# Optimization experiments

Hardware: AMD Instinct MI355X
Metric: run time of the kernel (lower is better)

## Reference

```python
import jax, jax.numpy as jnp
import numpy as np

GRID_SIZE = 5
SPLINE_ORDER = 3
GRID_RANGE = (-1.0, 1.0)
NUM_COEF = GRID_SIZE + SPLINE_ORDER  # 8


def make_grid(in_features):
    h = (GRID_RANGE[1] - GRID_RANGE[0]) / GRID_SIZE
    g = jnp.arange(-SPLINE_ORDER, GRID_SIZE + SPLINE_ORDER + 1, dtype=jnp.float32) * h + GRID_RANGE[0]
    return jnp.broadcast_to(g, (in_features, g.shape[0]))  # (in, grid_size + 2*order + 1)


def b_splines(x, grid):
    # x: (N, in); grid: (in, G). Cox-de Boor recursion -> (N, in, grid_size+order)
    xe = x[..., None]
    bases = ((xe >= grid[:, :-1]) & (xe < grid[:, 1:])).astype(x.dtype)
    for k in range(1, SPLINE_ORDER + 1):
        left = (xe - grid[:, : -(k + 1)]) / (grid[:, k:-1] - grid[:, : -(k + 1)])
        right = (grid[:, k + 1:] - xe) / (grid[:, k + 1:] - grid[:, 1:-k])
        bases = left * bases[..., :-1] + right * bases[..., 1:]
    return bases


def kan_linear(x, grid, base_w, spline_w, scaler):
    # base path: silu(x) @ base_w.T   (base_w: (out, in))
    base_out = jnp.einsum('ni,oi->no', jax.nn.silu(x), base_w)
    # spline path: flatten basis and scaled spline weights into one GEMM
    basis = b_splines(x, grid)                       # (N, in, 8)
    sw = spline_w * scaler[..., None]                # (out, in, 8)
    spline_out = jnp.einsum('nik,oik->no', basis, sw)
    return base_out + spline_out


def setup_inputs() -> dict:
    key = jax.random.key(0)
    ks = jax.random.split(key, 8)
    d = 1024
    dff = 4 * d
    n_tok = 4096
    s = 0.02
    return {
        'x': jax.random.normal(ks[0], (n_tok, d), dtype=jnp.float32),
        'base_w1': jax.random.normal(ks[1], (dff, d), dtype=jnp.float32) * s,
        'spline_w1': jax.random.normal(ks[2], (dff, d, NUM_COEF), dtype=jnp.float32) * s,
        'scaler1': jnp.ones((dff, d), dtype=jnp.float32),
        'base_w2': jax.random.normal(ks[3], (d, dff), dtype=jnp.float32) * s,
        'spline_w2': jax.random.normal(ks[4], (d, dff, NUM_COEF), dtype=jnp.float32) * s,
        'scaler2': jnp.ones((d, dff), dtype=jnp.float32),
        'grid1': make_grid(d),
        'grid2': make_grid(dff),
    }


def reference(x, base_w1, spline_w1, scaler1, base_w2, spline_w2, scaler2, grid1, grid2):
    h = kan_linear(x, grid1, base_w1, spline_w1, scaler1)
    h = jax.nn.gelu(h, approximate=False)  # torch nn.GELU default (erf)
    h = kan_linear(h, grid2, base_w2, spline_w2, scaler2)
    # Dropout(0.1) is identity in eval mode
    return h + x
```

## Files before the change

kernel.cpp:

```cpp
#include <hip/hip_runtime.h>
#include <hip/hip_fp16.h>

typedef _Float16 half_t;
typedef __attribute__((ext_vector_type(8))) _Float16 half8;
typedef __attribute__((ext_vector_type(4))) float f32x4;

#define AS1 __attribute__((address_space(1)))
#define AS3 __attribute__((address_space(3)))

__device__ __forceinline__ void gload16(const half_t* g, half_t* l) {
  __builtin_amdgcn_global_load_lds((const AS1 void*)g, (AS3 void*)l, 16, 0, 0);
}

__device__ __forceinline__ void bspline8u(float x, float out[8]) {
  float g[12];
#pragma unroll
  for (int j = 0; j < 12; ++j) g[j] = (float)(j - 3) * 0.4f - 1.0f;
  float b[11];
#pragma unroll
  for (int j = 0; j < 11; ++j)
    b[j] = (x >= g[j] && x < g[j + 1]) ? 1.0f : 0.0f;
#pragma unroll
  for (int k = 1; k <= 3; ++k) {
#pragma unroll
    for (int j = 0; j + k < 11; ++j) {
      float rl = 1.0f / (g[j + k] - g[j]);
      float rr = 1.0f / (g[j + k + 1] - g[j + 1]);
      b[j] = ((x - g[j]) * rl) * b[j] + ((g[j + k + 1] - x) * rr) * b[j + 1];
    }
  }
#pragma unroll
  for (int j = 0; j < 8; ++j) out[j] = b[j];
}

__global__ void wconv_kernel(const float* __restrict__ bw, const float* __restrict__ sw,
                             const float* __restrict__ sc, half_t* __restrict__ W,
                             int ibits, int ldw) {
  int idx = blockIdx.x * 256 + threadIdx.x;
  int o = idx >> ibits;
  int i = idx & ((1 << ibits) - 1);
  int c = i >> 10;
  int il = i & 1023;
  float b = bw[idx];
  float scv = sc[idx];
  const float4* svp = (const float4*)sw;
  float4 s0 = svp[(size_t)idx * 2];
  float4 s1 = svp[(size_t)idx * 2 + 1];
  half_t* wrow = W + (size_t)o * ldw + c * 9216;
  wrow[il] = (half_t)b;
  half8 hv;
  hv[0] = (half_t)(s0.x * scv); hv[1] = (half_t)(s0.y * scv);
  hv[2] = (half_t)(s0.z * scv); hv[3] = (half_t)(s0.w * scv);
  hv[4] = (half_t)(s1.x * scv); hv[5] = (half_t)(s1.y * scv);
  hv[6] = (half_t)(s1.z * scv); hv[7] = (half_t)(s1.w * scv);
  *(half8*)&wrow[1024 + il * 8] = hv;
}

template <typename ST>
__global__ void expand_kernel(const ST* __restrict__ src, half_t* __restrict__ dst,
                              int Isrc, int i0, int dsub, int kexp) {
  int idx = blockIdx.x * 256 + threadIdx.x;
  int n = idx >> 10;
  int il = idx & 1023;
  float v = (float)src[(size_t)n * Isrc + i0 + il];
  float bs[8];
  bspline8u(v, bs);
  half_t* drow = dst + (size_t)n * kexp + (size_t)dsub * 9216;
  drow[il] = (half_t)(v / (1.0f + expf(-v)));
  half8 hb;
#pragma unroll
  for (int k = 0; k < 8; ++k) hb[k] = (half_t)bs[k];
  *(half8*)&drow[1024 + il * 8] = hb;
}

#define STA(c, t, h)                                                          \
  {                                                                           \
    int r0_ = wid * 8 + (h) * 64;                                             \
    const half_t* g_ = Abase + (size_t)(r0_ + srow) * ldkA +                  \
                       (size_t)(t) * 64 + scol;                               \
    gload16(g_, &As[c][r0_ * 64]);                                            \
    gload16(g_ + (size_t)128 * ldkA, &As[c][(r0_ + 128) * 64]);               \
  }
#define STB(c, t, h)                                                          \
  {                                                                           \
    int r0_ = (wid >> 2) * 64 + (wid & 3) * 8 + (h) * 32;                     \
    const half_t* g_ = Bbase + (size_t)(r0_ + srow) * ldkB +                  \
                       (size_t)(t) * 64 + scol;                               \
    gload16(g_, &Bs[c][r0_ * 64]);                                            \
    gload16(g_ + (size_t)128 * ldkB, &Bs[c][(r0_ + 128) * 64]);               \
  }
#define PHASE(c, mh, nh, ...)                                                 \
  do {                                                                        \
    half8 af[4][2];                                                           \
    half8 bf[2][2];                                                           \
    _Pragma("unroll") for (int a = 0; a < 4; ++a) {                           \
      int row_ = wm * 128 + (mh) * 64 + a * 16 + (lane & 15);                 \
      _Pragma("unroll") for (int ks = 0; ks < 2; ++ks) {                      \
        int ch_ = (ks * 4 + (lane >> 4)) ^ (lane & 7);                        \
        af[a][ks] = *(const half8*)&As[c][row_ * 64 + ch_ * 8];               \
      }                                                                       \
    }                                                                         \
    _Pragma("unroll") for (int b = 0; b < 2; ++b) {                           \
      int row_ = wn * 64 + (nh) * 32 + b * 16 + (lane & 15);                  \
      _Pragma("unroll") for (int ks = 0; ks < 2; ++ks) {                      \
        int ch_ = (ks * 4 + (lane >> 4)) ^ (lane & 7);                        \
        bf[b][ks] = *(const half8*)&Bs[c][row_ * 64 + ch_ * 8];               \
      }                                                                       \
    }                                                                         \
    asm volatile("s_waitcnt vmcnt(6)" ::: "memory");                          \
    __VA_ARGS__                                                               \
    __builtin_amdgcn_s_barrier();                                             \
    __builtin_amdgcn_sched_barrier(0);                                        \
    __builtin_amdgcn_s_setprio(1);                                            \
    _Pragma("unroll") for (int ks = 0; ks < 2; ++ks)                          \
      _Pragma("unroll") for (int a = 0; a < 4; ++a)                           \
        _Pragma("unroll") for (int b = 0; b < 2; ++b)                         \
          acc[(mh) * 4 + a][(nh) * 2 + b] =                                   \
              __builtin_amdgcn_mfma_f32_16x16x32_f16(                         \
                  af[a][ks], bf[b][ks], acc[(mh) * 4 + a][(nh) * 2 + b],      \
                  0, 0, 0);                                                   \
    __builtin_amdgcn_s_setprio(0);                                            \
    __builtin_amdgcn_s_barrier();                                             \
    __builtin_amdgcn_sched_barrier(0);                                        \
  } while (0)

template <int MODE>
__global__ __launch_bounds__(512, 2) void gemm8_kernel(
    const half_t* __restrict__ A, const half_t* __restrict__ B,
    int ldkA, int ldkB, int kzLen,
    float* __restrict__ Cout, half_t* __restrict__ Hout, int ldc) {
  __shared__ __align__(16) half_t As[2][256 * 64];
  __shared__ __align__(16) half_t Bs[2][256 * 64];

  const int tid = threadIdx.x;
  const int wid = tid >> 6;
  const int lane = tid & 63;
  const int wm = wid >> 2;
  const int wn = wid & 3;

  const half_t* Abase = A + (size_t)blockIdx.x * 256 * ldkA +
                        (size_t)blockIdx.z * kzLen;
  const half_t* Bbase = B + (size_t)blockIdx.y * 256 * ldkB +
                        (size_t)blockIdx.z * kzLen;

  const int srow = lane >> 3;
  const int scol = ((lane & 7) ^ srow) * 8;

  const int nt = kzLen >> 6;

  f32x4 acc[8][4] = {};

  STA(0, 0, 0); STB(0, 0, 0); STB(0, 0, 1); STA(0, 0, 1);
  STA(1, 1, 0); STB(1, 1, 0);
  asm volatile("s_waitcnt vmcnt(0)" ::: "memory");
  __builtin_amdgcn_s_barrier();
  __builtin_amdgcn_sched_barrier(0);

  for (int i = 0; i < (nt >> 1); ++i) {
    const int t = 2 * i;
    const bool s2 = (t + 2 < nt);
    const bool s3 = (t + 3 < nt);
    PHASE(0, 0, 0, { STB(1, t + 1, 1); });
    PHASE(0, 0, 1, { STA(1, t + 1, 1); });
    PHASE(0, 1, 0, { if (s2) STA(0, t + 2, 0); });
    PHASE(0, 1, 1, { if (s2) STB(0, t + 2, 0); });
    PHASE(1, 0, 0, { if (s2) STB(0, t + 2, 1); });
    PHASE(1, 0, 1, { if (s2) STA(0, t + 2, 1); });
    PHASE(1, 1, 0, { if (s3) STA(1, t + 3, 0); });
    PHASE(1, 1, 1, { if (s3) STB(1, t + 3, 0); });
  }

  const int r_lo = (lane >> 4) << 2;
  const int col0 = (int)blockIdx.y * 256 + wn * 64 + (lane & 15);
  const int row00 = (int)blockIdx.x * 256 + wm * 128 + r_lo;
#pragma unroll
  for (int mf = 0; mf < 8; ++mf)
#pragma unroll
    for (int nf = 0; nf < 4; ++nf)
#pragma unroll
      for (int j = 0; j < 4; ++j) {
        float v = acc[mf][nf][j];
        size_t off = (size_t)(row00 + mf * 16 + j) * ldc + col0 + nf * 16;
        if constexpr (MODE == 0) {
          v = 0.5f * v * (1.0f + erff(v * 0.70710678118654752f));
          Hout[off] = (half_t)v;
        } else {
          atomicAdd(&Cout[off], v);
        }
      }
}

extern "C" void kernel_launch(void* const* d_in, const int* in_sizes, int n_in,
                              void* d_out, int out_size, void* d_ws, size_t ws_size,
                              hipStream_t stream) {
  const float* x   = (const float*)d_in[0];
  const float* bw1 = (const float*)d_in[1];
  const float* sw1 = (const float*)d_in[2];
  const float* sc1 = (const float*)d_in[3];
  const float* bw2 = (const float*)d_in[4];
  const float* sw2 = (const float*)d_in[5];
  const float* sc2 = (const float*)d_in[6];
  float* out = (float*)d_out;

  half_t* Wbuf = (half_t*)d_ws;
  const size_t W_HALVES = (size_t)4096 * 9216;
  const size_t A1_HALVES = (size_t)4096 * 9216;
  const size_t HH_HALVES = (size_t)4096 * 4096;
  int abuf_chunks = 1;
  if (ws_size >= (W_HALVES + A1_HALVES * 4 + HH_HALVES) * sizeof(half_t))
    abuf_chunks = 4;
  else if (ws_size >= (W_HALVES + A1_HALVES * 2 + HH_HALVES) * sizeof(half_t))
    abuf_chunks = 2;
  half_t* Abuf = Wbuf + W_HALVES;
  half_t* Hh   = Abuf + A1_HALVES * abuf_chunks;

  const int T = 256;
  const int NB = (4096 * 1024) / T;

  hipMemcpyAsync(out, x, (size_t)4096 * 1024 * sizeof(float),
                 hipMemcpyDeviceToDevice, stream);

  wconv_kernel<<<NB, T, 0, stream>>>(bw1, sw1, sc1, Wbuf, 10, 9216);
  expand_kernel<float><<<NB, T, 0, stream>>>(x, Abuf, 1024, 0, 0, 9216);
  gemm8_kernel<0><<<dim3(16, 16, 1), 512, 0, stream>>>(
      Abuf, Wbuf, 9216, 9216, 9216, nullptr, Hh, 4096);

  wconv_kernel<<<NB, T, 0, stream>>>(bw2, sw2, sc2, Wbuf, 12, 36864);
  if (abuf_chunks == 4) {
    for (int c = 0; c < 4; ++c)
      expand_kernel<half_t><<<NB, T, 0, stream>>>(Hh, Abuf, 4096, c * 1024, c, 36864);
    gemm8_kernel<4><<<dim3(16, 4, 4), 512, 0, stream>>>(
        Abuf, Wbuf, 36864, 36864, 9216, out, nullptr, 1024);
  } else if (abuf_chunks == 2) {
    for (int c = 0; c < 2; ++c) {
      expand_kernel<half_t><<<NB, T, 0, stream>>>(Hh, Abuf, 4096, c * 2048, 0, 18432);
      expand_kernel<half_t><<<NB, T, 0, stream>>>(Hh, Abuf, 4096, c * 2048 + 1024, 1, 18432);
      gemm8_kernel<4><<<dim3(16, 4, 4), 512, 0, stream>>>(
          Abuf, Wbuf + (size_t)c * 18432, 18432, 36864, 4608, out, nullptr, 1024);
    }
  } else {
    for (int c = 0; c < 4; ++c) {
      expand_kernel<half_t><<<NB, T, 0, stream>>>(Hh, Abuf, 4096, c * 1024, 0, 9216);
      gemm8_kernel<4><<<dim3(16, 4, 4), 512, 0, stream>>>(
          Abuf, Wbuf + (size_t)c * 9216, 9216, 36864, 2304, out, nullptr, 1024);
    }
  }
}
```

Before: 868.0 us.

## Reuse A/B register fragments across GEMM phases with serpentine ordering and peeled tail

The per-phase LDS reads are restructured so each phase loads only the fragments it newly needs. A fragments are kept across nh phases and two B fragment sets are kept across mh phases, visited in a serpentine order (00,01,11,10). This is meant to cut LDS read traffic per K-tile roughly in half. The final iteration is peeled with tapering vmcnt waits so the s2/s3 conditionals leave the steady-state loop. The extra live half8 registers raise register pressure under the 512-thread, 2-block launch bounds, and the vmcnt accounting in the peeled tail must be exact.

```diff
diff --git a/kernel.cpp b/kernel.cpp
--- a/kernel.cpp
+++ b/kernel.cpp
@@ -89,26 +89,27 @@
     gload16(g_, &Bs[c][r0_ * 64]);                                            \
     gload16(g_ + (size_t)128 * ldkB, &Bs[c][(r0_ + 128) * 64]);               \
   }
-#define PHASE(c, mh, nh, ...)                                                 \
+#define LOADAF(c, mh)                                                         \
+  _Pragma("unroll") for (int a = 0; a < 4; ++a) {                             \
+    int row_ = wm * 128 + (mh) * 64 + a * 16 + (lane & 15);                   \
+    _Pragma("unroll") for (int ks = 0; ks < 2; ++ks) {                        \
+      int ch_ = (ks * 4 + (lane >> 4)) ^ (lane & 7);                          \
+      af[a][ks] = *(const half8*)&As[c][row_ * 64 + ch_ * 8];                 \
+    }                                                                         \
+  }
+#define LOADBF(c, nh, bfv)                                                    \
+  _Pragma("unroll") for (int b = 0; b < 2; ++b) {                             \
+    int row_ = wn * 64 + (nh) * 32 + b * 16 + (lane & 15);                    \
+    _Pragma("unroll") for (int ks = 0; ks < 2; ++ks) {                        \
+      int ch_ = (ks * 4 + (lane >> 4)) ^ (lane & 7);                          \
+      bfv[b][ks] = *(const half8*)&Bs[c][row_ * 64 + ch_ * 8];                \
+    }                                                                         \
+  }
+#define DOPHASE(W, mh, nh, bfv, LOADS, STAGE)                                 \
   do {                                                                        \
-    half8 af[4][2];                                                           \
-    half8 bf[2][2];                                                           \
-    _Pragma("unroll") for (int a = 0; a < 4; ++a) {                           \
-      int row_ = wm * 128 + (mh) * 64 + a * 16 + (lane & 15);                 \
-      _Pragma("unroll") for (int ks = 0; ks < 2; ++ks) {                      \
-        int ch_ = (ks * 4 + (lane >> 4)) ^ (lane & 7);                        \
-        af[a][ks] = *(const half8*)&As[c][row_ * 64 + ch_ * 8];               \
-      }                                                                       \
-    }                                                                         \
-    _Pragma("unroll") for (int b = 0; b < 2; ++b) {                           \
-      int row_ = wn * 64 + (nh) * 32 + b * 16 + (lane & 15);                  \
-      _Pragma("unroll") for (int ks = 0; ks < 2; ++ks) {                      \
-        int ch_ = (ks * 4 + (lane >> 4)) ^ (lane & 7);                        \
-        bf[b][ks] = *(const half8*)&Bs[c][row_ * 64 + ch_ * 8];               \
-      }                                                                       \
-    }                                                                         \
-    asm volatile("s_waitcnt vmcnt(6)" ::: "memory");                          \
-    __VA_ARGS__                                                               \
+    LOADS                                                                     \
+    STAGE                                                                     \
+    asm volatile("s_waitcnt vmcnt(" #W ")" ::: "memory");                     \
     __builtin_amdgcn_s_barrier();                                             \
     __builtin_amdgcn_sched_barrier(0);                                        \
     __builtin_amdgcn_s_setprio(1);                                            \
@@ -117,7 +118,7 @@
         _Pragma("unroll") for (int b = 0; b < 2; ++b)                         \
           acc[(mh) * 4 + a][(nh) * 2 + b] =                                   \
               __builtin_amdgcn_mfma_f32_16x16x32_f16(                         \
-                  af[a][ks], bf[b][ks], acc[(mh) * 4 + a][(nh) * 2 + b],      \
+                  af[a][ks], bfv[b][ks], acc[(mh) * 4 + a][(nh) * 2 + b],     \
                   0, 0, 0);                                                   \
     __builtin_amdgcn_s_setprio(0);                                            \
     __builtin_amdgcn_s_barrier();                                             \
@@ -149,6 +150,7 @@
   const int nt = kzLen >> 6;
 
   f32x4 acc[8][4] = {};
+  half8 af[4][2], bA[2][2], bB[2][2];
 
   STA(0, 0, 0); STB(0, 0, 0); STB(0, 0, 1); STA(0, 0, 1);
   STA(1, 1, 0); STB(1, 1, 0);
@@ -156,18 +158,27 @@
   __builtin_amdgcn_s_barrier();
   __builtin_amdgcn_sched_barrier(0);
 
-  for (int i = 0; i < (nt >> 1); ++i) {
+  for (int i = 0; i < (nt >> 1) - 1; ++i) {
     const int t = 2 * i;
-    const bool s2 = (t + 2 < nt);
-    const bool s3 = (t + 3 < nt);
-    PHASE(0, 0, 0, { STB(1, t + 1, 1); });
-    PHASE(0, 0, 1, { STA(1, t + 1, 1); });
-    PHASE(0, 1, 0, { if (s2) STA(0, t + 2, 0); });
-    PHASE(0, 1, 1, { if (s2) STB(0, t + 2, 0); });
-    PHASE(1, 0, 0, { if (s2) STB(0, t + 2, 1); });
-    PHASE(1, 0, 1, { if (s2) STA(0, t + 2, 1); });
-    PHASE(1, 1, 0, { if (s3) STA(1, t + 3, 0); });
-    PHASE(1, 1, 1, { if (s3) STB(1, t + 3, 0); });
+    DOPHASE(6, 0, 0, bA, { LOADAF(0, 0) LOADBF(0, 0, bA) }, { STB(1, t + 1, 1); });
+    DOPHASE(6, 0, 1, bB, { LOADBF(0, 1, bB) },              { STA(1, t + 1, 1); });
+    DOPHASE(6, 1, 1, bB, { LOADAF(0, 1) },                  { STA(0, t + 2, 0); });
+    DOPHASE(6, 1, 0, bA, {},                                { STB(0, t + 2, 0); });
+    DOPHASE(6, 0, 0, bA, { LOADAF(1, 0) LOADBF(1, 0, bA) }, { STB(0, t + 2, 1); });
+    DOPHASE(6, 0, 1, bB, { LOADBF(1, 1, bB) },              { STA(0, t + 2, 1); });
+    DOPHASE(6, 1, 1, bB, { LOADAF(1, 1) },                  { STA(1, t + 3, 0); });
+    DOPHASE(6, 1, 0, bA, {},                                { STB(1, t + 3, 0); });
+  }
+  {
+    const int t = nt - 2;
+    DOPHASE(6, 0, 0, bA, { LOADAF(0, 0) LOADBF(0, 0, bA) }, { STB(1, t + 1, 1); });
+    DOPHASE(6, 0, 1, bB, { LOADBF(0, 1, bB) },              { STA(1, t + 1, 1); });
+    DOPHASE(6, 1, 1, bB, { LOADAF(0, 1) },                  {});
+    DOPHASE(6, 1, 0, bA, {},                                {});
+    DOPHASE(4, 0, 0, bA, { LOADAF(1, 0) LOADBF(1, 0, bA) }, {});
+    DOPHASE(2, 0, 1, bB, { LOADBF(1, 1, bB) },              {});
+    DOPHASE(0, 1, 1, bB, { LOADAF(1, 1) },                  {});
+    DOPHASE(0, 1, 0, bA, {},                                {});
   }
 
   const int r_lo = (lane >> 4) << 2;
```

Result: faster. 821.5 us (-5.4%).
